# Performance work log

Hardware: AMD Instinct MI355X
Metric: run time of the kernel (lower is better)

The kernel has to match this reference:

```python
import jax, jax.numpy as jnp
import numpy as np

N, F, H, T, E, HOR = 50000, 24, 128, 12, 800000, 6


def setup_inputs() -> dict:
    key = jax.random.key(0)
    ks = jax.random.split(key, 16)
    x_seq = jax.random.normal(ks[0], (T, N, F), jnp.float32)
    ei_seq = jax.random.randint(ks[1], (T, 2, E), 0, N, jnp.int32)
    ea_seq = jax.random.uniform(ks[2], (T, E), jnp.float32)
    mask_seq = jax.random.bernoulli(ks[3], 0.9, (T, N))
    s = 1.0 / float(np.sqrt(H))
    def w(k, shape):
        return jax.random.uniform(k, shape, jnp.float32, -s, s)
    params = dict(
        Wz=w(ks[4], (F, H)), Wr=w(ks[5], (F, H)), Wh=w(ks[6], (F, H)),
        bz=jnp.zeros((H,), jnp.float32), br=jnp.zeros((H,), jnp.float32), bh=jnp.zeros((H,), jnp.float32),
        LWz=w(ks[7], (2 * H, H)), LWr=w(ks[8], (2 * H, H)), LWh=w(ks[9], (2 * H, H)),
        Lbz=w(ks[10], (H,)), Lbr=w(ks[11], (H,)), Lbh=w(ks[12], (H,)),
        headW=w(ks[13], (H, F)), headb=w(ks[14], (F,)),
    )
    return dict(x_seq=x_seq, ei_seq=ei_seq, ea_seq=ea_seq, mask_seq=mask_seq, id_seq=0, **params)


def _gcn(x, src, dst, ew, W, b):
    xw = x @ W                                                     # [N,H]
    deg = jnp.zeros((x.shape[0],), xw.dtype).at[dst].add(ew) + 1.0  # in-degree + self-loop
    dinv = jax.lax.rsqrt(deg)
    coef = dinv[src] * ew * dinv[dst]                              # [E]
    agg = jnp.zeros_like(xw).at[dst].add(xw[src] * coef[:, None])
    return agg + xw * (1.0 / deg)[:, None] + b                     # normalized self-loop term


def _cell(x, src, dst, ew, h, p):
    # TGCN (GCN-GRU) cell from pytorch_geometric_temporal
    z = jax.nn.sigmoid(jnp.concatenate([_gcn(x, src, dst, ew, p['Wz'], p['bz']), h], 1) @ p['LWz'] + p['Lbz'])
    r = jax.nn.sigmoid(jnp.concatenate([_gcn(x, src, dst, ew, p['Wr'], p['br']), h], 1) @ p['LWr'] + p['Lbr'])
    htil = jnp.tanh(jnp.concatenate([_gcn(x, src, dst, ew, p['Wh'], p['bh']), h * r], 1) @ p['LWh'] + p['Lbh'])
    return z * h + (1.0 - z) * htil


def _forward(x_seq, ei_seq, ea_seq, mask_seq, p):
    Nn, Hh = x_seq.shape[1], p['LWz'].shape[1]

    # Encoder over T steps: h_store keeps last hidden of every node ever present
    def enc(carry, inp):
        h_store, seen = carry
        x, ei, ew, mask = inp
        h_prev = jnp.where((mask & seen)[:, None], h_store, 0.0)
        h_new = _cell(x, ei[0], ei[1], ew, h_prev, p)
        return (jnp.where(mask[:, None], h_new, h_store), seen | mask), None

    init = (jnp.zeros((Nn, Hh), x_seq.dtype), jnp.zeros((Nn,), bool))
    (h_store, seen), _ = jax.lax.scan(enc, init, (x_seq, ei_seq, ea_seq, mask_seq))

    h_prev = jnp.where((mask_seq[-1] & seen)[:, None], h_store, 0.0)
    src_l, dst_l, ew_l = ei_seq[-1, 0], ei_seq[-1, 1], ea_seq[-1]

    def dec(carry, _):
        h, inp = carry
        h_new = _cell(inp, src_l, dst_l, ew_l, h, p)
        y = h_new @ p['headW'] + p['headb']
        return (h_new, y), y

    _, preds = jax.lax.scan(dec, (h_prev, x_seq[-1]), None, length=HOR)
    return preds  # [horizon, N, out_channels]


def reference(x_seq, ei_seq, ea_seq, mask_seq, id_seq, Wz, Wr, Wh, bz, br, bh,
              LWz, LWr, LWh, Lbz, Lbr, Lbh, headW, headb):
    p = dict(Wz=Wz, Wr=Wr, Wh=Wh, bz=bz, br=br, bh=bh,
             LWz=LWz, LWr=LWr, LWh=LWh, Lbz=Lbz, Lbr=Lbr, Lbh=Lbh,
             headW=headW, headb=headb)
    return _forward(x_seq, ei_seq, ea_seq, mask_seq, p)
```

## Files before the change

### kernel.cpp

```cpp
#include <hip/hip_runtime.h>

#define NN 50000
#define FF 24
#define HH 128
#define TT 12
#define EE 800000
#define HORZ 6


__global__ void k_maskdetect(const unsigned char* __restrict__ m, int* __restrict__ flag) {
    int i = blockIdx.x * 256 + threadIdx.x;
    if (i < 16384 && (i & 3) != 0 && m[i] != 0) atomicOr(flag, 1);
}

__global__ void k_maskconv(const unsigned char* __restrict__ mraw, const int* __restrict__ flag,
                           unsigned char* __restrict__ mout) {
    int i = blockIdx.x * 256 + threadIdx.x;
    if (i >= TT * NN) return;
    if (*flag) mout[i] = (mraw[i] != 0);
    else       mout[i] = (((const int*)mraw)[i] != 0);
}


__global__ void k_hist(const int* __restrict__ ei, int* __restrict__ cnt) {
    int idx = blockIdx.x * 256 + threadIdx.x;
    if (idx >= TT * EE) return;
    int t = idx / EE, e = idx - t * EE;
    int dst = ei[((size_t)t * 2 + 1) * EE + e];
    atomicAdd(&cnt[t * NN + dst], 1);
}

__global__ void k_scan(const int* __restrict__ cnt, int* __restrict__ offs,
                       int* __restrict__ cursor) {
    __shared__ int sums[1024];
    int t = blockIdx.x, tid = threadIdx.x;
    const int per = (NN + 1023) / 1024;
    int base = tid * per;
    int s = 0;
    for (int i = 0; i < per; i++) {
        int idx = base + i;
        if (idx < NN) s += cnt[t * NN + idx];
    }
    sums[tid] = s;
    __syncthreads();
    for (int off = 1; off < 1024; off <<= 1) {
        int tv = (tid >= off) ? sums[tid - off] : 0;
        __syncthreads();
        sums[tid] += tv;
        __syncthreads();
    }
    int run = sums[tid] - s;
    for (int i = 0; i < per; i++) {
        int idx = base + i;
        if (idx < NN) {
            offs[t * (NN + 1) + idx] = run;
            cursor[t * NN + idx] = run;
            run += cnt[t * NN + idx];
        }
    }
    if (tid == 1023) offs[t * (NN + 1) + NN] = sums[1023];
}

__global__ void k_fill(const int* __restrict__ ei, const float* __restrict__ ea,
                       int* __restrict__ cursor, int2* __restrict__ edges) {
    int idx = blockIdx.x * 256 + threadIdx.x;
    if (idx >= TT * EE) return;
    int t = idx / EE, e = idx - t * EE;
    int dst = ei[((size_t)t * 2 + 1) * EE + e];
    int src = ei[((size_t)t * 2 + 0) * EE + e];
    int pos = atomicAdd(&cursor[t * NN + dst], 1);
    edges[(size_t)t * EE + pos] = make_int2(src, __float_as_int(ea[(size_t)t * EE + e]));
}

__global__ void k_degdinv(const int* __restrict__ offs, const int2* __restrict__ edges,
                          float* __restrict__ dinv) {
    int idx = blockIdx.x * 256 + threadIdx.x;
    if (idx >= TT * NN) return;
    int t = idx / NN, n = idx - t * NN;
    int b = offs[t * (NN + 1) + n], en = offs[t * (NN + 1) + n + 1];
    float s = 0.f;
    for (int j = b; j < en; j++) s += __int_as_float(edges[(size_t)t * EE + j].y);
    dinv[idx] = rsqrtf(s + 1.0f);
}

__global__ void k_coef(const int* __restrict__ offs, const float* __restrict__ dinv,
                       int2* __restrict__ edges) {
    int idx = blockIdx.x * 256 + threadIdx.x;
    if (idx >= TT * NN) return;
    int t = idx / NN, n = idx - t * NN;
    int b = offs[t * (NN + 1) + n], en = offs[t * (NN + 1) + n + 1];
    float di = dinv[idx];
    for (int j = b; j < en; j++) {
        int2 p = edges[(size_t)t * EE + j];
        float v = __int_as_float(p.y) * di * dinv[t * NN + p.x];
        edges[(size_t)t * EE + j].y = __float_as_int(v);
    }
}


__global__ void k_fold(const float* __restrict__ Wz, const float* __restrict__ Wr,
                       const float* __restrict__ Wh,
                       const float* __restrict__ bz, const float* __restrict__ br,
                       const float* __restrict__ bh,
                       const float* __restrict__ LWz, const float* __restrict__ LWr,
                       const float* __restrict__ LWh,
                       const float* __restrict__ Lbz, const float* __restrict__ Lbr,
                       const float* __restrict__ Lbh,
                       float* __restrict__ Call, float* __restrict__ b2) {
    int g = blockIdx.x, c = threadIdx.x;
    const float* W  = g == 0 ? Wz : (g == 1 ? Wr : Wh);
    const float* LW = g == 0 ? LWz : (g == 1 ? LWr : LWh);
    const float* bg = g == 0 ? bz : (g == 1 ? br : bh);
    const float* Lb = g == 0 ? Lbz : (g == 1 ? Lbr : Lbh);
    for (int j = 0; j < FF; j++) {
        float a = 0.f;
        for (int k = 0; k < HH; k++) a += W[j * HH + k] * LW[k * HH + c];
        Call[((size_t)g * FF + j) * HH + c] = a;
    }
    float a = Lb[c];
    for (int k = 0; k < HH; k++) a += bg[k] * LW[k * HH + c];
    b2[g * HH + c] = a;
}


__global__ void k_gather(const float* __restrict__ x, const int* __restrict__ offs,
                         const int2* __restrict__ edges,
                         const float* __restrict__ dinv, float* __restrict__ xe) {
    int idx = blockIdx.x * 256 + threadIdx.x;
    if (idx >= NN * FF) return;
    int n = idx / FF, f = idx - n * FF;
    int b = offs[n], en = offs[n + 1];
    float di = dinv[n];
    float acc = x[idx] * di * di;
    for (int j = b; j < en; j++) {
        int2 p = edges[j];
        acc += x[p.x * FF + f] * __int_as_float(p.y);
    }
    xe[idx] = acc;
}


#define FMA8X2(SARR, M0, K)                                                                  \
    {                                                                                        \
        float4 v_;                                                                           \
        v_ = *(const float4*)&SARR[M0 + 0][K];                                               \
        az0 += v_.x*wz0 + v_.y*wz1 + v_.z*wz2 + v_.w*wz3;                                    \
        ar0 += v_.x*wr0 + v_.y*wr1 + v_.z*wr2 + v_.w*wr3;                                    \
        v_ = *(const float4*)&SARR[M0 + 1][K];                                               \
        az1 += v_.x*wz0 + v_.y*wz1 + v_.z*wz2 + v_.w*wz3;                                    \
        ar1 += v_.x*wr0 + v_.y*wr1 + v_.z*wr2 + v_.w*wr3;                                    \
        v_ = *(const float4*)&SARR[M0 + 2][K];                                               \
        az2 += v_.x*wz0 + v_.y*wz1 + v_.z*wz2 + v_.w*wz3;                                    \
        ar2 += v_.x*wr0 + v_.y*wr1 + v_.z*wr2 + v_.w*wr3;                                    \
        v_ = *(const float4*)&SARR[M0 + 3][K];                                               \
        az3 += v_.x*wz0 + v_.y*wz1 + v_.z*wz2 + v_.w*wz3;                                    \
        ar3 += v_.x*wr0 + v_.y*wr1 + v_.z*wr2 + v_.w*wr3;                                    \
        v_ = *(const float4*)&SARR[M0 + 4][K];                                               \
        az4 += v_.x*wz0 + v_.y*wz1 + v_.z*wz2 + v_.w*wz3;                                    \
        ar4 += v_.x*wr0 + v_.y*wr1 + v_.z*wr2 + v_.w*wr3;                                    \
        v_ = *(const float4*)&SARR[M0 + 5][K];                                               \
        az5 += v_.x*wz0 + v_.y*wz1 + v_.z*wz2 + v_.w*wz3;                                    \
        ar5 += v_.x*wr0 + v_.y*wr1 + v_.z*wr2 + v_.w*wr3;                                    \
        v_ = *(const float4*)&SARR[M0 + 6][K];                                               \
        az6 += v_.x*wz0 + v_.y*wz1 + v_.z*wz2 + v_.w*wz3;                                    \
        ar6 += v_.x*wr0 + v_.y*wr1 + v_.z*wr2 + v_.w*wr3;                                    \
        v_ = *(const float4*)&SARR[M0 + 7][K];                                               \
        az7 += v_.x*wz0 + v_.y*wz1 + v_.z*wz2 + v_.w*wz3;                                    \
        ar7 += v_.x*wr0 + v_.y*wr1 + v_.z*wr2 + v_.w*wr3;                                    \
    }

#define FMA8X(SARR, M0, K)                                                        \
    {                                                                             \
        float4 v_;                                                                \
        v_ = *(const float4*)&SARR[M0 + 0][K]; a0 += v_.x*w0 + v_.y*w1 + v_.z*w2 + v_.w*w3; \
        v_ = *(const float4*)&SARR[M0 + 1][K]; a1 += v_.x*w0 + v_.y*w1 + v_.z*w2 + v_.w*w3; \
        v_ = *(const float4*)&SARR[M0 + 2][K]; a2 += v_.x*w0 + v_.y*w1 + v_.z*w2 + v_.w*w3; \
        v_ = *(const float4*)&SARR[M0 + 3][K]; a3 += v_.x*w0 + v_.y*w1 + v_.z*w2 + v_.w*w3; \
        v_ = *(const float4*)&SARR[M0 + 4][K]; a4 += v_.x*w0 + v_.y*w1 + v_.z*w2 + v_.w*w3; \
        v_ = *(const float4*)&SARR[M0 + 5][K]; a5 += v_.x*w0 + v_.y*w1 + v_.z*w2 + v_.w*w3; \
        v_ = *(const float4*)&SARR[M0 + 6][K]; a6 += v_.x*w0 + v_.y*w1 + v_.z*w2 + v_.w*w3; \
        v_ = *(const float4*)&SARR[M0 + 7][K]; a7 += v_.x*w0 + v_.y*w1 + v_.z*w2 + v_.w*w3; \
    }

template <int DOHEAD>
__global__ __launch_bounds__(256) void k_cell(
        const float* __restrict__ xe, const float* __restrict__ hin,
        const unsigned char* __restrict__ gmask,
        const float* __restrict__ Call, const float* __restrict__ b2,
        const float* __restrict__ LWz, const float* __restrict__ LWr,
        const float* __restrict__ LWh,
        const unsigned char* __restrict__ wmask, float* __restrict__ hout,
        const float* __restrict__ headW, const float* __restrict__ headb,
        float* __restrict__ y) {
    __shared__ float s_xe[16][FF];
    __shared__ float s_h0[16][HH];
    __shared__ float s_z[16][HH];
    __shared__ float s_hr[16][HH];
    int nb = blockIdx.x * 16;
    int tid = threadIdx.x;

    for (int i = tid; i < 16 * FF; i += 256) {
        s_xe[i / FF][i % FF] = xe[(size_t)nb * FF + i];
    }
    for (int i = tid; i < 16 * HH; i += 256) {
        int m = i >> 7, k = i & 127;
        float v = hin[((size_t)nb + m) * HH + k];
        if (gmask && !gmask[nb + m]) v = 0.f;
        s_h0[m][k] = v;
    }
    __syncthreads();

    int g = tid >> 7, c = tid & 127;
    int m0 = g * 8;

    {
        const float* Cz   = Call;
        const float* Cr   = Call + (size_t)FF * HH;
        const float* LWzb = LWz + (size_t)HH * HH;
        const float* LWrb = LWr + (size_t)HH * HH;
        float bbz = b2[c], bbr = b2[HH + c];
        float az0 = bbz, az1 = bbz, az2 = bbz, az3 = bbz, az4 = bbz, az5 = bbz, az6 = bbz, az7 = bbz;
        float ar0 = bbr, ar1 = bbr, ar2 = bbr, ar3 = bbr, ar4 = bbr, ar5 = bbr, ar6 = bbr, ar7 = bbr;
#pragma unroll
        for (int k = 0; k < FF; k += 4) {
            float wz0 = Cz[(k + 0) * HH + c], wz1 = Cz[(k + 1) * HH + c];
            float wz2 = Cz[(k + 2) * HH + c], wz3 = Cz[(k + 3) * HH + c];
            float wr0 = Cr[(k + 0) * HH + c], wr1 = Cr[(k + 1) * HH + c];
            float wr2 = Cr[(k + 2) * HH + c], wr3 = Cr[(k + 3) * HH + c];
            FMA8X2(s_xe, m0, k);
        }
#pragma unroll 4
        for (int k = 0; k < HH; k += 4) {
            float wz0 = LWzb[(k + 0) * HH + c], wz1 = LWzb[(k + 1) * HH + c];
            float wz2 = LWzb[(k + 2) * HH + c], wz3 = LWzb[(k + 3) * HH + c];
            float wr0 = LWrb[(k + 0) * HH + c], wr1 = LWrb[(k + 1) * HH + c];
            float wr2 = LWrb[(k + 2) * HH + c], wr3 = LWrb[(k + 3) * HH + c];
            FMA8X2(s_h0, m0, k);
        }
#pragma unroll
        for (int r = 0; r < 8; r++) {
            float az = (r == 0) ? az0 : (r == 1) ? az1 : (r == 2) ? az2 : (r == 3) ? az3
                     : (r == 4) ? az4 : (r == 5) ? az5 : (r == 6) ? az6 : az7;
            float ar = (r == 0) ? ar0 : (r == 1) ? ar1 : (r == 2) ? ar2 : (r == 3) ? ar3
                     : (r == 4) ? ar4 : (r == 5) ? ar5 : (r == 6) ? ar6 : ar7;
            s_z[m0 + r][c]  = 1.f / (1.f + __expf(-az));
            s_hr[m0 + r][c] = (1.f / (1.f + __expf(-ar))) * s_h0[m0 + r][c];
        }
    }
    __syncthreads();

    {
        const float* Ch   = Call + (size_t)2 * FF * HH;
        const float* LWhb = LWh + (size_t)HH * HH;
        float bb = b2[2 * HH + c];
        float a0 = bb, a1 = bb, a2 = bb, a3 = bb, a4 = bb, a5 = bb, a6 = bb, a7 = bb;
#pragma unroll
        for (int k = 0; k < FF; k += 4) {
            float w0 = Ch[(k + 0) * HH + c], w1 = Ch[(k + 1) * HH + c];
            float w2 = Ch[(k + 2) * HH + c], w3 = Ch[(k + 3) * HH + c];
            FMA8X(s_xe, m0, k);
        }
#pragma unroll 4
        for (int k = 0; k < HH; k += 4) {
            float w0 = LWhb[(k + 0) * HH + c], w1 = LWhb[(k + 1) * HH + c];
            float w2 = LWhb[(k + 2) * HH + c], w3 = LWhb[(k + 3) * HH + c];
            FMA8X(s_hr, m0, k);
        }
#pragma unroll
        for (int r = 0; r < 8; r++) {
            float a = (r == 0) ? a0 : (r == 1) ? a1 : (r == 2) ? a2 : (r == 3) ? a3
                    : (r == 4) ? a4 : (r == 5) ? a5 : (r == 6) ? a6 : a7;
            int m = m0 + r;
            float e2 = __expf(2.f * a);
            float ht = 1.f - 2.f / (e2 + 1.f);
            float z = s_z[m][c];
            float h0v = s_h0[m][c];
            float hn = z * h0v + (1.f - z) * ht;
            int n = nb + m;
            if (wmask) {
                if (wmask[n]) hout[(size_t)n * HH + c] = hn;
            } else {
                hout[(size_t)n * HH + c] = hn;
            }
            if (DOHEAD) s_z[m][c] = hn;
        }
    }

    if (DOHEAD) {
        __syncthreads();
        for (int i = tid; i < 16 * FF; i += 256) {
            int m = i / FF, f = i - m * FF;
            float acc = headb[f];
#pragma unroll 8
            for (int cJ = 0; cJ < HH; cJ++) acc += s_z[m][cJ] * headW[cJ * FF + f];
            y[(size_t)nb * FF + i] = acc;
        }
    }
}

extern "C" void kernel_launch(void* const* d_in, const int* in_sizes, int n_in,
                              void* d_out, int out_size, void* d_ws, size_t ws_size,
                              hipStream_t stream) {
    const float* x_seq = (const float*)d_in[0];
    const int*   ei    = (const int*)d_in[1];
    const float* ea    = (const float*)d_in[2];
    const unsigned char* mraw = (const unsigned char*)d_in[3];
    const float* Wz  = (const float*)d_in[5];
    const float* Wr  = (const float*)d_in[6];
    const float* Wh  = (const float*)d_in[7];
    const float* bz  = (const float*)d_in[8];
    const float* br  = (const float*)d_in[9];
    const float* bh  = (const float*)d_in[10];
    const float* LWz = (const float*)d_in[11];
    const float* LWr = (const float*)d_in[12];
    const float* LWh = (const float*)d_in[13];
    const float* Lbz = (const float*)d_in[14];
    const float* Lbr = (const float*)d_in[15];
    const float* Lbh = (const float*)d_in[16];
    const float* headW = (const float*)d_in[17];
    const float* headb = (const float*)d_in[18];
    float* out = (float*)d_out;

    char* wp = (char*)d_ws;
    int*   cnt    = (int*)wp;   wp += sizeof(int) * TT * NN;
    int*   cursor = (int*)wp;   wp += sizeof(int) * TT * NN;
    int*   offs   = (int*)wp;   wp += sizeof(int) * TT * (NN + 1);
    int2*  edges  = (int2*)wp;  wp += sizeof(int2) * (size_t)TT * EE;
    float* dinv   = (float*)wp; wp += sizeof(float) * TT * NN;
    float* hstore = (float*)wp; wp += sizeof(float) * (size_t)NN * HH;
    float* hp     = (float*)wp; wp += sizeof(float) * (size_t)NN * HH;
    float* xebuf  = (float*)wp; wp += sizeof(float) * NN * FF;
    float* Call   = (float*)wp; wp += sizeof(float) * 3 * FF * HH;
    float* b2     = (float*)wp; wp += sizeof(float) * 3 * HH;
    int*   mflag  = (int*)wp;   wp += 256;
    unsigned char* mask = (unsigned char*)wp; wp += TT * NN;
    if (ws_size < (size_t)(wp - (char*)d_ws)) return;

    hipMemsetAsync(mflag, 0, sizeof(int), stream);
    k_maskdetect<<<64, 256, 0, stream>>>(mraw, mflag);
    k_maskconv<<<(TT * NN + 255) / 256, 256, 0, stream>>>(mraw, mflag, mask);

    hipMemsetAsync(cnt, 0, sizeof(int) * TT * NN, stream);
    hipMemsetAsync(hstore, 0, sizeof(float) * NN * HH, stream);
    k_hist<<<(TT * EE + 255) / 256, 256, 0, stream>>>(ei, cnt);
    k_scan<<<TT, 1024, 0, stream>>>(cnt, offs, cursor);
    k_fill<<<(TT * EE + 255) / 256, 256, 0, stream>>>(ei, ea, cursor, edges);
    k_degdinv<<<(TT * NN + 255) / 256, 256, 0, stream>>>(offs, edges, dinv);
    k_coef<<<(TT * NN + 255) / 256, 256, 0, stream>>>(offs, dinv, edges);
    k_fold<<<3, 128, 0, stream>>>(Wz, Wr, Wh, bz, br, bh, LWz, LWr, LWh, Lbz, Lbr, Lbh, Call, b2);

    for (int t = 0; t < TT; t++) {
        const float* xt = x_seq + (size_t)t * NN * FF;
        const unsigned char* mt = mask + (size_t)t * NN;
        k_gather<<<(NN * FF + 255) / 256, 256, 0, stream>>>(
            xt, offs + t * (NN + 1), edges + (size_t)t * EE, dinv + t * NN, xebuf);
        k_cell<0><<<NN / 16, 256, 0, stream>>>(
            xebuf, hstore, mt, Call, b2, LWz, LWr, LWh, mt, hstore,
            nullptr, nullptr, nullptr);
    }

    const int*  offsl  = offs + (TT - 1) * (NN + 1);
    const int2* edgesl = edges + (size_t)(TT - 1) * EE;
    const float* dil   = dinv + (TT - 1) * NN;
    for (int k = 0; k < HORZ; k++) {
        const float* xin = (k == 0) ? (x_seq + (size_t)(TT - 1) * NN * FF)
                                    : (out + (size_t)(k - 1) * NN * FF);
        k_gather<<<(NN * FF + 255) / 256, 256, 0, stream>>>(
            xin, offsl, edgesl, dil, xebuf);
        k_cell<1><<<NN / 16, 256, 0, stream>>>(
            xebuf, (k == 0) ? hstore : hp,
            (k == 0) ? (mask + (size_t)(TT - 1) * NN) : nullptr,
            Call, b2, LWz, LWr, LWh, nullptr, hp,
            headW, headb, out + (size_t)k * NN * FF);
    }
}
```

Baseline: 5.121 ms.

## Retile GRU cell to 32 rows, vectorize gather, precompute CSR ranks

The cell kernel now handles 32 nodes per block, with each thread computing two output columns for eight rows. This doubles register reuse of weights loaded from global memory, and the z gate stays in registers instead of shared memory. The gather kernel assigns half a node's 24 features to each thread and reads them as float4 vectors, so each edge index is read once rather than once per feature. CSR construction saves the atomic rank from the histogram pass, so the fill pass needs no second atomic. The cost is an extra TT*EE int buffer and higher register pressure in the cell kernel.

```diff
diff --git a/kernel.cpp b/kernel.cpp
--- a/kernel.cpp
+++ b/kernel.cpp
@@ -6,6 +6,9 @@
 #define TT 12
 #define EE 800000
 #define HORZ 6
+#define BR 32
+
+__device__ __forceinline__ float sigmf(float a) { return 1.f / (1.f + __expf(-a)); }
 
 
 __global__ void k_maskdetect(const unsigned char* __restrict__ m, int* __restrict__ flag) {
@@ -22,16 +25,16 @@
 }
 
 
-__global__ void k_hist(const int* __restrict__ ei, int* __restrict__ cnt) {
+__global__ void k_hist(const int* __restrict__ ei, int* __restrict__ cnt,
+                       int* __restrict__ rank) {
     int idx = blockIdx.x * 256 + threadIdx.x;
     if (idx >= TT * EE) return;
     int t = idx / EE, e = idx - t * EE;
     int dst = ei[((size_t)t * 2 + 1) * EE + e];
-    atomicAdd(&cnt[t * NN + dst], 1);
-}
-
-__global__ void k_scan(const int* __restrict__ cnt, int* __restrict__ offs,
-                       int* __restrict__ cursor) {
+    rank[idx] = atomicAdd(&cnt[t * NN + dst], 1);
+}
+
+__global__ void k_scan(const int* __restrict__ cnt, int* __restrict__ offs) {
     __shared__ int sums[1024];
     int t = blockIdx.x, tid = threadIdx.x;
     const int per = (NN + 1023) / 1024;
@@ -54,7 +57,6 @@
         int idx = base + i;
         if (idx < NN) {
             offs[t * (NN + 1) + idx] = run;
-            cursor[t * NN + idx] = run;
             run += cnt[t * NN + idx];
         }
     }
@@ -62,13 +64,14 @@
 }
 
 __global__ void k_fill(const int* __restrict__ ei, const float* __restrict__ ea,
-                       int* __restrict__ cursor, int2* __restrict__ edges) {
+                       const int* __restrict__ offs, const int* __restrict__ rank,
+                       int2* __restrict__ edges) {
     int idx = blockIdx.x * 256 + threadIdx.x;
     if (idx >= TT * EE) return;
     int t = idx / EE, e = idx - t * EE;
     int dst = ei[((size_t)t * 2 + 1) * EE + e];
     int src = ei[((size_t)t * 2 + 0) * EE + e];
-    int pos = atomicAdd(&cursor[t * NN + dst], 1);
+    int pos = offs[t * (NN + 1) + dst] + rank[idx];
     edges[(size_t)t * EE + pos] = make_int2(src, __float_as_int(ea[(size_t)t * EE + e]));
 }
 
@@ -124,63 +127,37 @@
 
 
 __global__ void k_gather(const float* __restrict__ x, const int* __restrict__ offs,
-                         const int2* __restrict__ edges,
-                         const float* __restrict__ dinv, float* __restrict__ xe) {
+                         const int2* __restrict__ edges, const float* __restrict__ dinv,
+                         float* __restrict__ xe) {
     int idx = blockIdx.x * 256 + threadIdx.x;
-    if (idx >= NN * FF) return;
-    int n = idx / FF, f = idx - n * FF;
+    if (idx >= NN * 2) return;
+    int n = idx >> 1, h = idx & 1;
     int b = offs[n], en = offs[n + 1];
-    float di = dinv[n];
-    float acc = x[idx] * di * di;
+    float di = dinv[n], sc = di * di;
+    const float* xb = x + (size_t)n * FF + h * 12;
+    float4 a0 = *(const float4*)(xb + 0);
+    float4 a1 = *(const float4*)(xb + 4);
+    float4 a2 = *(const float4*)(xb + 8);
+    a0.x *= sc; a0.y *= sc; a0.z *= sc; a0.w *= sc;
+    a1.x *= sc; a1.y *= sc; a1.z *= sc; a1.w *= sc;
+    a2.x *= sc; a2.y *= sc; a2.z *= sc; a2.w *= sc;
     for (int j = b; j < en; j++) {
         int2 p = edges[j];
-        acc += x[p.x * FF + f] * __int_as_float(p.y);
-    }
-    xe[idx] = acc;
-}
-
-
-#define FMA8X2(SARR, M0, K)                                                                  \
-    {                                                                                        \
-        float4 v_;                                                                           \
-        v_ = *(const float4*)&SARR[M0 + 0][K];                                               \
-        az0 += v_.x*wz0 + v_.y*wz1 + v_.z*wz2 + v_.w*wz3;                                    \
-        ar0 += v_.x*wr0 + v_.y*wr1 + v_.z*wr2 + v_.w*wr3;                                    \
-        v_ = *(const float4*)&SARR[M0 + 1][K];                                               \
-        az1 += v_.x*wz0 + v_.y*wz1 + v_.z*wz2 + v_.w*wz3;                                    \
-        ar1 += v_.x*wr0 + v_.y*wr1 + v_.z*wr2 + v_.w*wr3;                                    \
-        v_ = *(const float4*)&SARR[M0 + 2][K];                                               \
-        az2 += v_.x*wz0 + v_.y*wz1 + v_.z*wz2 + v_.w*wz3;                                    \
-        ar2 += v_.x*wr0 + v_.y*wr1 + v_.z*wr2 + v_.w*wr3;                                    \
-        v_ = *(const float4*)&SARR[M0 + 3][K];                                               \
-        az3 += v_.x*wz0 + v_.y*wz1 + v_.z*wz2 + v_.w*wz3;                                    \
-        ar3 += v_.x*wr0 + v_.y*wr1 + v_.z*wr2 + v_.w*wr3;                                    \
-        v_ = *(const float4*)&SARR[M0 + 4][K];                                               \
-        az4 += v_.x*wz0 + v_.y*wz1 + v_.z*wz2 + v_.w*wz3;                                    \
-        ar4 += v_.x*wr0 + v_.y*wr1 + v_.z*wr2 + v_.w*wr3;                                    \
-        v_ = *(const float4*)&SARR[M0 + 5][K];                                               \
-        az5 += v_.x*wz0 + v_.y*wz1 + v_.z*wz2 + v_.w*wz3;                                    \
-        ar5 += v_.x*wr0 + v_.y*wr1 + v_.z*wr2 + v_.w*wr3;                                    \
-        v_ = *(const float4*)&SARR[M0 + 6][K];                                               \
-        az6 += v_.x*wz0 + v_.y*wz1 + v_.z*wz2 + v_.w*wz3;                                    \
-        ar6 += v_.x*wr0 + v_.y*wr1 + v_.z*wr2 + v_.w*wr3;                                    \
-        v_ = *(const float4*)&SARR[M0 + 7][K];                                               \
-        az7 += v_.x*wz0 + v_.y*wz1 + v_.z*wz2 + v_.w*wz3;                                    \
-        ar7 += v_.x*wr0 + v_.y*wr1 + v_.z*wr2 + v_.w*wr3;                                    \
-    }
-
-#define FMA8X(SARR, M0, K)                                                        \
-    {                                                                             \
-        float4 v_;                                                                \
-        v_ = *(const float4*)&SARR[M0 + 0][K]; a0 += v_.x*w0 + v_.y*w1 + v_.z*w2 + v_.w*w3; \
-        v_ = *(const float4*)&SARR[M0 + 1][K]; a1 += v_.x*w0 + v_.y*w1 + v_.z*w2 + v_.w*w3; \
-        v_ = *(const float4*)&SARR[M0 + 2][K]; a2 += v_.x*w0 + v_.y*w1 + v_.z*w2 + v_.w*w3; \
-        v_ = *(const float4*)&SARR[M0 + 3][K]; a3 += v_.x*w0 + v_.y*w1 + v_.z*w2 + v_.w*w3; \
-        v_ = *(const float4*)&SARR[M0 + 4][K]; a4 += v_.x*w0 + v_.y*w1 + v_.z*w2 + v_.w*w3; \
-        v_ = *(const float4*)&SARR[M0 + 5][K]; a5 += v_.x*w0 + v_.y*w1 + v_.z*w2 + v_.w*w3; \
-        v_ = *(const float4*)&SARR[M0 + 6][K]; a6 += v_.x*w0 + v_.y*w1 + v_.z*w2 + v_.w*w3; \
-        v_ = *(const float4*)&SARR[M0 + 7][K]; a7 += v_.x*w0 + v_.y*w1 + v_.z*w2 + v_.w*w3; \
-    }
+        float w = __int_as_float(p.y);
+        const float* xs = x + (size_t)p.x * FF + h * 12;
+        float4 v0 = *(const float4*)(xs + 0);
+        float4 v1 = *(const float4*)(xs + 4);
+        float4 v2 = *(const float4*)(xs + 8);
+        a0.x += v0.x * w; a0.y += v0.y * w; a0.z += v0.z * w; a0.w += v0.w * w;
+        a1.x += v1.x * w; a1.y += v1.y * w; a1.z += v1.z * w; a1.w += v1.w * w;
+        a2.x += v2.x * w; a2.y += v2.y * w; a2.z += v2.z * w; a2.w += v2.w * w;
+    }
+    float* o = xe + (size_t)n * FF + h * 12;
+    *(float4*)(o + 0) = a0;
+    *(float4*)(o + 4) = a1;
+    *(float4*)(o + 8) = a2;
+}
+
 
 template <int DOHEAD>
 __global__ __launch_bounds__(256) void k_cell(
@@ -192,59 +169,90 @@
         const unsigned char* __restrict__ wmask, float* __restrict__ hout,
         const float* __restrict__ headW, const float* __restrict__ headb,
         float* __restrict__ y) {
-    __shared__ float s_xe[16][FF];
-    __shared__ float s_h0[16][HH];
-    __shared__ float s_z[16][HH];
-    __shared__ float s_hr[16][HH];
-    int nb = blockIdx.x * 16;
+    __shared__ float s_xe[BR][FF];
+    __shared__ float s_h0[BR][HH];
+    __shared__ float s_hr[BR][HH];
+    int nb = blockIdx.x * BR;
     int tid = threadIdx.x;
 
-    for (int i = tid; i < 16 * FF; i += 256) {
-        s_xe[i / FF][i % FF] = xe[(size_t)nb * FF + i];
-    }
-    for (int i = tid; i < 16 * HH; i += 256) {
+    for (int i = tid; i < BR * FF; i += 256) {
+        int m = i / FF, f = i - m * FF;
+        int n = nb + m;
+        s_xe[m][f] = (n < NN) ? xe[(size_t)n * FF + f] : 0.f;
+    }
+    for (int i = tid; i < BR * HH; i += 256) {
         int m = i >> 7, k = i & 127;
-        float v = hin[((size_t)nb + m) * HH + k];
-        if (gmask && !gmask[nb + m]) v = 0.f;
+        int n = nb + m;
+        float v = 0.f;
+        if (n < NN) {
+            v = hin[(size_t)n * HH + k];
+            if (gmask && !gmask[n]) v = 0.f;
+        }
         s_h0[m][k] = v;
     }
     __syncthreads();
 
-    int g = tid >> 7, c = tid & 127;
-    int m0 = g * 8;
+    int c2 = tid & 63, rh = tid >> 6;
+    int m0 = rh * 8;
+    int cA = c2, cB = c2 + 64;
+
+    float zz[8][2];
 
     {
         const float* Cz   = Call;
         const float* Cr   = Call + (size_t)FF * HH;
         const float* LWzb = LWz + (size_t)HH * HH;
         const float* LWrb = LWr + (size_t)HH * HH;
-        float bbz = b2[c], bbr = b2[HH + c];
-        float az0 = bbz, az1 = bbz, az2 = bbz, az3 = bbz, az4 = bbz, az5 = bbz, az6 = bbz, az7 = bbz;
-        float ar0 = bbr, ar1 = bbr, ar2 = bbr, ar3 = bbr, ar4 = bbr, ar5 = bbr, ar6 = bbr, ar7 = bbr;
+        float az[8][2], ar[8][2];
+        float bzA = b2[cA], bzB = b2[cB], brA = b2[HH + cA], brB = b2[HH + cB];
+#pragma unroll
+        for (int r = 0; r < 8; r++) {
+            az[r][0] = bzA; az[r][1] = bzB; ar[r][0] = brA; ar[r][1] = brB;
+        }
 #pragma unroll
         for (int k = 0; k < FF; k += 4) {
-            float wz0 = Cz[(k + 0) * HH + c], wz1 = Cz[(k + 1) * HH + c];
-            float wz2 = Cz[(k + 2) * HH + c], wz3 = Cz[(k + 3) * HH + c];
-            float wr0 = Cr[(k + 0) * HH + c], wr1 = Cr[(k + 1) * HH + c];
-            float wr2 = Cr[(k + 2) * HH + c], wr3 = Cr[(k + 3) * HH + c];
-            FMA8X2(s_xe, m0, k);
-        }
-#pragma unroll 4
+            float wz0A = Cz[(k + 0) * HH + cA], wz1A = Cz[(k + 1) * HH + cA];
+            float wz2A = Cz[(k + 2) * HH + cA], wz3A = Cz[(k + 3) * HH + cA];
+            float wz0B = Cz[(k + 0) * HH + cB], wz1B = Cz[(k + 1) * HH + cB];
+            float wz2B = Cz[(k + 2) * HH + cB], wz3B = Cz[(k + 3) * HH + cB];
+            float wr0A = Cr[(k + 0) * HH + cA], wr1A = Cr[(k + 1) * HH + cA];
+            float wr2A = Cr[(k + 2) * HH + cA], wr3A = Cr[(k + 3) * HH + cA];
+            float wr0B = Cr[(k + 0) * HH + cB], wr1B = Cr[(k + 1) * HH + cB];
+            float wr2B = Cr[(k + 2) * HH + cB], wr3B = Cr[(k + 3) * HH + cB];
+#pragma unroll
+            for (int r = 0; r < 8; r++) {
+                float4 v = *(const float4*)&s_xe[m0 + r][k];
+                az[r][0] += v.x * wz0A + v.y * wz1A + v.z * wz2A + v.w * wz3A;
+                az[r][1] += v.x * wz0B + v.y * wz1B + v.z * wz2B + v.w * wz3B;
+                ar[r][0] += v.x * wr0A + v.y * wr1A + v.z * wr2A + v.w * wr3A;
+                ar[r][1] += v.x * wr0B + v.y * wr1B + v.z * wr2B + v.w * wr3B;
+            }
+        }
+#pragma unroll 2
         for (int k = 0; k < HH; k += 4) {
-            float wz0 = LWzb[(k + 0) * HH + c], wz1 = LWzb[(k + 1) * HH + c];
-            float wz2 = LWzb[(k + 2) * HH + c], wz3 = LWzb[(k + 3) * HH + c];
-            float wr0 = LWrb[(k + 0) * HH + c], wr1 = LWrb[(k + 1) * HH + c];
-            float wr2 = LWrb[(k + 2) * HH + c], wr3 = LWrb[(k + 3) * HH + c];
-            FMA8X2(s_h0, m0, k);
+            float wz0A = LWzb[(k + 0) * HH + cA], wz1A = LWzb[(k + 1) * HH + cA];
+            float wz2A = LWzb[(k + 2) * HH + cA], wz3A = LWzb[(k + 3) * HH + cA];
+            float wz0B = LWzb[(k + 0) * HH + cB], wz1B = LWzb[(k + 1) * HH + cB];
+            float wz2B = LWzb[(k + 2) * HH + cB], wz3B = LWzb[(k + 3) * HH + cB];
+            float wr0A = LWrb[(k + 0) * HH + cA], wr1A = LWrb[(k + 1) * HH + cA];
+            float wr2A = LWrb[(k + 2) * HH + cA], wr3A = LWrb[(k + 3) * HH + cA];
+            float wr0B = LWrb[(k + 0) * HH + cB], wr1B = LWrb[(k + 1) * HH + cB];
+            float wr2B = LWrb[(k + 2) * HH + cB], wr3B = LWrb[(k + 3) * HH + cB];
+#pragma unroll
+            for (int r = 0; r < 8; r++) {
+                float4 v = *(const float4*)&s_h0[m0 + r][k];
+                az[r][0] += v.x * wz0A + v.y * wz1A + v.z * wz2A + v.w * wz3A;
+                az[r][1] += v.x * wz0B + v.y * wz1B + v.z * wz2B + v.w * wz3B;
+                ar[r][0] += v.x * wr0A + v.y * wr1A + v.z * wr2A + v.w * wr3A;
+                ar[r][1] += v.x * wr0B + v.y * wr1B + v.z * wr2B + v.w * wr3B;
+            }
         }
 #pragma unroll
         for (int r = 0; r < 8; r++) {
-            float az = (r == 0) ? az0 : (r == 1) ? az1 : (r == 2) ? az2 : (r == 3) ? az3
-                     : (r == 4) ? az4 : (r == 5) ? az5 : (r == 6) ? az6 : az7;
-            float ar = (r == 0) ? ar0 : (r == 1) ? ar1 : (r == 2) ? ar2 : (r == 3) ? ar3
-                     : (r == 4) ? ar4 : (r == 5) ? ar5 : (r == 6) ? ar6 : ar7;
-            s_z[m0 + r][c]  = 1.f / (1.f + __expf(-az));
-            s_hr[m0 + r][c] = (1.f / (1.f + __expf(-ar))) * s_h0[m0 + r][c];
+            zz[r][0] = sigmf(az[r][0]);
+            zz[r][1] = sigmf(az[r][1]);
+            s_hr[m0 + r][cA] = sigmf(ar[r][0]) * s_h0[m0 + r][cA];
+            s_hr[m0 + r][cB] = sigmf(ar[r][1]) * s_h0[m0 + r][cB];
         }
     }
     __syncthreads();
@@ -252,48 +260,68 @@
     {
         const float* Ch   = Call + (size_t)2 * FF * HH;
         const float* LWhb = LWh + (size_t)HH * HH;
-        float bb = b2[2 * HH + c];
-        float a0 = bb, a1 = bb, a2 = bb, a3 = bb, a4 = bb, a5 = bb, a6 = bb, a7 = bb;
+        float ah[8][2];
+        float bhA = b2[2 * HH + cA], bhB = b2[2 * HH + cB];
+#pragma unroll
+        for (int r = 0; r < 8; r++) { ah[r][0] = bhA; ah[r][1] = bhB; }
 #pragma unroll
         for (int k = 0; k < FF; k += 4) {
-            float w0 = Ch[(k + 0) * HH + c], w1 = Ch[(k + 1) * HH + c];
-            float w2 = Ch[(k + 2) * HH + c], w3 = Ch[(k + 3) * HH + c];
-            FMA8X(s_xe, m0, k);
-        }
-#pragma unroll 4
+            float w0A = Ch[(k + 0) * HH + cA], w1A = Ch[(k + 1) * HH + cA];
+            float w2A = Ch[(k + 2) * HH + cA], w3A = Ch[(k + 3) * HH + cA];
+            float w0B = Ch[(k + 0) * HH + cB], w1B = Ch[(k + 1) * HH + cB];
+            float w2B = Ch[(k + 2) * HH + cB], w3B = Ch[(k + 3) * HH + cB];
+#pragma unroll
+            for (int r = 0; r < 8; r++) {
+                float4 v = *(const float4*)&s_xe[m0 + r][k];
+                ah[r][0] += v.x * w0A + v.y * w1A + v.z * w2A + v.w * w3A;
+                ah[r][1] += v.x * w0B + v.y * w1B + v.z * w2B + v.w * w3B;
+            }
+        }
+#pragma unroll 2
         for (int k = 0; k < HH; k += 4) {
-            float w0 = LWhb[(k + 0) * HH + c], w1 = LWhb[(k + 1) * HH + c];
-            float w2 = LWhb[(k + 2) * HH + c], w3 = LWhb[(k + 3) * HH + c];
-            FMA8X(s_hr, m0, k);
+            float w0A = LWhb[(k + 0) * HH + cA], w1A = LWhb[(k + 1) * HH + cA];
+            float w2A = LWhb[(k + 2) * HH + cA], w3A = LWhb[(k + 3) * HH + cA];
+            float w0B = LWhb[(k + 0) * HH + cB], w1B = LWhb[(k + 1) * HH + cB];
+            float w2B = LWhb[(k + 2) * HH + cB], w3B = LWhb[(k + 3) * HH + cB];
+#pragma unroll
+            for (int r = 0; r < 8; r++) {
+                float4 v = *(const float4*)&s_hr[m0 + r][k];
+                ah[r][0] += v.x * w0A + v.y * w1A + v.z * w2A + v.w * w3A;
+                ah[r][1] += v.x * w0B + v.y * w1B + v.z * w2B + v.w * w3B;
+            }
         }
 #pragma unroll
         for (int r = 0; r < 8; r++) {
-            float a = (r == 0) ? a0 : (r == 1) ? a1 : (r == 2) ? a2 : (r == 3) ? a3
-                    : (r == 4) ? a4 : (r == 5) ? a5 : (r == 6) ? a6 : a7;
-            int m = m0 + r;
-            float e2 = __expf(2.f * a);
-            float ht = 1.f - 2.f / (e2 + 1.f);
-            float z = s_z[m][c];
-            float h0v = s_h0[m][c];
-            float hn = z * h0v + (1.f - z) * ht;
-            int n = nb + m;
-            if (wmask) {
-                if (wmask[n]) hout[(size_t)n * HH + c] = hn;
-            } else {
-                hout[(size_t)n * HH + c] = hn;
-            }
-            if (DOHEAD) s_z[m][c] = hn;
+            int m = m0 + r, n = nb + m;
+            float e2A = __expf(2.f * ah[r][0]);
+            float e2B = __expf(2.f * ah[r][1]);
+            float htA = 1.f - 2.f / (e2A + 1.f);
+            float htB = 1.f - 2.f / (e2B + 1.f);
+            float h0A = s_h0[m][cA], h0B = s_h0[m][cB];
+            float hnA = zz[r][0] * h0A + (1.f - zz[r][0]) * htA;
+            float hnB = zz[r][1] * h0B + (1.f - zz[r][1]) * htB;
+            if (n < NN && (!wmask || wmask[n])) {
+                hout[(size_t)n * HH + cA] = hnA;
+                hout[(size_t)n * HH + cB] = hnB;
+            }
+            if (DOHEAD) { s_h0[m][cA] = hnA; s_h0[m][cB] = hnB; }
         }
     }
 
     if (DOHEAD) {
         __syncthreads();
-        for (int i = tid; i < 16 * FF; i += 256) {
+        for (int i = tid; i < BR * FF; i += 256) {
             int m = i / FF, f = i - m * FF;
+            int n = nb + m;
+            if (n >= NN) continue;
             float acc = headb[f];
 #pragma unroll 8
-            for (int cJ = 0; cJ < HH; cJ++) acc += s_z[m][cJ] * headW[cJ * FF + f];
-            y[(size_t)nb * FF + i] = acc;
+            for (int cJ = 0; cJ < HH; cJ += 4) {
+                float4 hv = *(const float4*)&s_h0[m][cJ];
+                acc += hv.x * headW[(cJ + 0) * FF + f] + hv.y * headW[(cJ + 1) * FF + f]
+                     + hv.z * headW[(cJ + 2) * FF + f] + hv.w * headW[(cJ + 3) * FF + f];
+            }
+            y[(size_t)n * FF + f] = acc;
         }
     }
 }
@@ -323,8 +351,8 @@
 
     char* wp = (char*)d_ws;
     int*   cnt    = (int*)wp;   wp += sizeof(int) * TT * NN;
-    int*   cursor = (int*)wp;   wp += sizeof(int) * TT * NN;
     int*   offs   = (int*)wp;   wp += sizeof(int) * TT * (NN + 1);
+    int*   rank   = (int*)wp;   wp += sizeof(int) * (size_t)TT * EE;
     int2*  edges  = (int2*)wp;  wp += sizeof(int2) * (size_t)TT * EE;
     float* dinv   = (float*)wp; wp += sizeof(float) * TT * NN;
     float* hstore = (float*)wp; wp += sizeof(float) * (size_t)NN * HH;
@@ -342,19 +370,21 @@
 
     hipMemsetAsync(cnt, 0, sizeof(int) * TT * NN, stream);
     hipMemsetAsync(hstore, 0, sizeof(float) * NN * HH, stream);
-    k_hist<<<(TT * EE + 255) / 256, 256, 0, stream>>>(ei, cnt);
-    k_scan<<<TT, 1024, 0, stream>>>(cnt, offs, cursor);
-    k_fill<<<(TT * EE + 255) / 256, 256, 0, stream>>>(ei, ea, cursor, edges);
+    k_hist<<<(TT * EE + 255) / 256, 256, 0, stream>>>(ei, cnt, rank);
+    k_scan<<<TT, 1024, 0, stream>>>(cnt, offs);
+    k_fill<<<(TT * EE + 255) / 256, 256, 0, stream>>>(ei, ea, offs, rank, edges);
     k_degdinv<<<(TT * NN + 255) / 256, 256, 0, stream>>>(offs, edges, dinv);
     k_coef<<<(TT * NN + 255) / 256, 256, 0, stream>>>(offs, dinv, edges);
     k_fold<<<3, 128, 0, stream>>>(Wz, Wr, Wh, bz, br, bh, LWz, LWr, LWh, Lbz, Lbr, Lbh, Call, b2);
 
+    const int cellGrid = (NN + BR - 1) / BR;
+
     for (int t = 0; t < TT; t++) {
         const float* xt = x_seq + (size_t)t * NN * FF;
         const unsigned char* mt = mask + (size_t)t * NN;
-        k_gather<<<(NN * FF + 255) / 256, 256, 0, stream>>>(
+        k_gather<<<(NN * 2 + 255) / 256, 256, 0, stream>>>(
             xt, offs + t * (NN + 1), edges + (size_t)t * EE, dinv + t * NN, xebuf);
-        k_cell<0><<<NN / 16, 256, 0, stream>>>(
+        k_cell<0><<<cellGrid, 256, 0, stream>>>(
             xebuf, hstore, mt, Call, b2, LWz, LWr, LWh, mt, hstore,
             nullptr, nullptr, nullptr);
     }
@@ -365,9 +395,9 @@
     for (int k = 0; k < HORZ; k++) {
         const float* xin = (k == 0) ? (x_seq + (size_t)(TT - 1) * NN * FF)
                                     : (out + (size_t)(k - 1) * NN * FF);
-        k_gather<<<(NN * FF + 255) / 256, 256, 0, stream>>>(
+        k_gather<<<(NN * 2 + 255) / 256, 256, 0, stream>>>(
             xin, offsl, edgesl, dil, xebuf);
-        k_cell<1><<<NN / 16, 256, 0, stream>>>(
+        k_cell<1><<<cellGrid, 256, 0, stream>>>(
             xebuf, (k == 0) ? hstore : hp,
             (k == 0) ? (mask + (size_t)(TT - 1) * NN) : nullptr,
             Call, b2, LWz, LWr, LWh, nullptr, hp,
```

Measured after the change: 6.489 ms. 26.7% more time.
